# Kernel optimization log

Hardware: AMD Instinct MI355X
Metric: run time of the kernel (lower is better)

The kernel has to match this reference:

```python
import jax, jax.numpy as jnp
import numpy as np
import math

IMAGE_SIZE = 256
N_ANGLES = 180


def setup_inputs() -> dict:
    key = jax.random.key(0)
    x = jax.random.normal(key, (4, 1, IMAGE_SIZE, IMAGE_SIZE), dtype=jnp.float32)
    return {"x": x}


def reference(x) -> jnp.ndarray:
    # Radon transform, circle=True: mask to inscribed circle, then for each
    # angle bilinearly sample the image along rotated coordinates
    # (torch.grid_sample, align_corners=True, zeros padding) and sum along rays.
    B = x.shape[0]
    S = IMAGE_SIZE
    A = N_ANGLES
    img = x.reshape(B, S, S)

    # circular mask (matches torch: sqrt(dist2) <= center with center = S//2)
    center = S // 2
    yy, xx = jnp.meshgrid(jnp.arange(S), jnp.arange(S), indexing='ij')
    dist = jnp.sqrt(((xx - center) ** 2 + (yy - center) ** 2).astype(jnp.float32))
    img = img * (dist <= center).astype(img.dtype)
    img_flat = img.reshape(B, S * S)

    # projection coordinates: meshgrid('ij') of linspace(-S/2, S/2, S)
    lin = jnp.linspace(-S / 2.0, S / 2.0, S, dtype=jnp.float32)
    X, Y = jnp.meshgrid(lin, lin, indexing='ij')  # [S,S]; X varies along i
    Xf, Yf = X.ravel(), Y.ravel()                 # [S*S]

    # all rotation angles at once: torch.linspace(0, 180, A) degrees
    ang = jnp.linspace(0.0, 180.0, A, dtype=jnp.float32) * (math.pi / 180.0)
    c = jnp.cos(ang)[:, None]  # [A,1]
    s = jnp.sin(ang)[:, None]
    half = S / 2.0
    gx = (c * Xf - s * Yf) / half  # [A, S*S], normalized grid x (width)
    gy = (s * Xf + c * Yf) / half  # [A, S*S], normalized grid y (height)

    # align_corners=True: pixel = (g + 1)/2 * (S - 1)
    px = (gx + 1.0) * 0.5 * (S - 1)
    py = (gy + 1.0) * 0.5 * (S - 1)

    x0 = jnp.floor(px)
    y0 = jnp.floor(py)
    wx = px - x0
    wy = py - y0
    x0i = x0.astype(jnp.int32)
    y0i = y0.astype(jnp.int32)
    x1i = x0i + 1
    y1i = y0i + 1

    def corner(xi, yi, w):
        # zeros padding: out-of-bounds corners contribute 0
        valid = (xi >= 0) & (xi < S) & (yi >= 0) & (yi < S)
        idx = jnp.clip(yi, 0, S - 1) * S + jnp.clip(xi, 0, S - 1)  # [A, S*S]
        vals = jnp.take(img_flat, idx, axis=1)                      # [B, A, S*S]
        return vals * (w * valid.astype(img.dtype))

    acc = (corner(x0i, y0i, (1.0 - wx) * (1.0 - wy))
           + corner(x1i, y0i, wx * (1.0 - wy))
           + corner(x0i, y1i, (1.0 - wx) * wy)
           + corner(x1i, y1i, wx * wy))  # [B, A, S*S]

    # flat order is (i, j) from meshgrid('ij'); torch sums over output H == i
    sinogram = acc.reshape(B, A, S, S).sum(axis=2)  # [B, A, S]
    return sinogram
```

## Files before the change

### kernel.cpp

```cpp
#include <hip/hip_runtime.h>
#include <hip/hip_fp16.h>
#include <math.h>

#define S 256
#define A 180
#define B 4
#define PMAX 310
#define NROWS 264

__global__ void radon_mask_f16(const float* __restrict__ in, __half* __restrict__ out) {
    int idx = blockIdx.x * 256 + threadIdx.x;
    int p = idx & (S * S - 1);
    int y = p >> 8;
    int x = p & 255;
    int dx = x - 128, dy = y - 128;
    float v = in[idx];
    v = (dx * dx + dy * dy <= 16384) ? v : 0.0f;
    out[idx] = __float2half(v);
}

__global__ __launch_bounds__(1024, 1) void radon_lds_kernel(const __half* __restrict__ img,
                                                            float* __restrict__ out) {
    __shared__ __half lds[NROWS * PMAX];

    const int a = blockIdx.x;
    const int b = blockIdx.y;
    const int tid = threadIdx.x;

    float ang = (float)a * (float)(M_PI / 179.0);
    float sn, cs;
    sincosf(ang, &sn, &cs);

    int P = 264;
    {
        float best = 1e9f;
        for (int cand = 264; cand <= PMAX; cand += 2) {
            float sd = 0.5f * fabsf((float)cand * cs - sn);
            float m = sd - 2.0f * floorf(sd * 0.5f);
            float score = fabsf(m - 1.0f);
            if (score < best) { best = score; P = cand; }
        }
    }
    const int Ph = P >> 1;

    uint* l32 = (uint*)lds;
    const uint* __restrict__ src = (const uint*)(img + (size_t)b * (S * S));
#pragma unroll
    for (int k = 0; k < 32; ++k) {
        int p = k * 1024 + tid;
        int y = p >> 7;
        int xd = p & 127;
        l32[(y + 4) * Ph + xd + 2] = src[p];
    }
    {
        int rsel = tid >> 7;
        int r = (rsel < 4) ? rsel : (256 + rsel);
        l32[r * Ph + (tid & 127) + 4] = 0u;
        if (tid < 32) {
            int rs = tid >> 2;
            int rr = (rs < 4) ? rs : (256 + rs);
            l32[rr * Ph + (tid & 3)] = 0u;
        }
        int rc = 4 + (tid >> 2);
        int dsel = tid & 3;
        int dd = (dsel < 2) ? dsel : (128 + dsel);
        l32[rc * Ph + dd] = 0u;
    }
    __syncthreads();

    const int j = tid >> 2;
    const int q = tid & 3;

    const float ry = (float)j - 127.5f;
    const float bx = fmaf(-sn, ry, 127.5f);
    const float by = fmaf(cs, ry, 127.5f);
    const float ry2 = ry * ry;

    float h = sqrtf(16934.0f - ry2);
    int ilo = max((int)ceilf(127.5f - h), 0);
    int ihi = min((int)floorf(127.5f + h) + 1, S);
    int len = ihi - ilo;
    int lo = ilo + ((q * len) >> 2);
    int hi = ilo + (((q + 1) * len) >> 2);

    const __half* __restrict__ orig = &lds[4 * P + 4];

    float acc = 0.0f;

#pragma unroll 4
    for (int i = lo; i < hi; ++i) {
        float rx = (float)i - 127.5f;
        float px = fmaf(cs, rx, bx);
        float py = fmaf(sn, rx, by);

        float x0f = floorf(px);
        float y0f = floorf(py);
        float wx = px - x0f;
        float wy = py - y0f;
        int x0 = (int)x0f;
        int y0 = (int)y0f;
        float ux = 1.0f - wx;
        float uy = 1.0f - wy;
        float w00 = ux * uy;
        float w10 = wx * uy;
        float w01 = ux * wy;
        float w11 = wx * wy;

        const __half* p0 = orig + (y0 * P + x0);
        float v00 = __half2float(p0[0]);
        float v10 = __half2float(p0[1]);
        float v01 = __half2float(p0[P]);
        float v11 = __half2float(p0[P + 1]);

        acc = fmaf(w00, v00, fmaf(w10, v10, fmaf(w01, v01, fmaf(w11, v11, acc))));
    }

    __syncthreads();
    float* red = (float*)lds;
    red[tid] = acc;
    __syncthreads();
    if (tid < 256) {
        float4 v = ((const float4*)red)[tid];
        out[((size_t)b * A + a) * S + tid] = v.x + v.y + v.z + v.w;
    }
}

extern "C" void kernel_launch(void* const* d_in, const int* in_sizes, int n_in,
                              void* d_out, int out_size, void* d_ws, size_t ws_size,
                              hipStream_t stream) {
    const float* x = (const float*)d_in[0];
    float* out = (float*)d_out;
    __half* masked = (__half*)d_ws;

    radon_mask_f16<<<dim3((B * S * S) / 256), dim3(256), 0, stream>>>(x, masked);
    radon_lds_kernel<<<dim3(A, B), dim3(1024), 0, stream>>>(masked, out);
}
```

Baseline: 96.03 us.

## Split image into two row halves per block to shrink LDS and raise occupancy

Each (angle, batch) block is split into two blocks along grid z, and each block loads only about half the image rows into LDS. Every ray is cut at the row-128 crossing, each half sums its own segment, and the two partial sums are combined with atomicAdd into an output that the mask kernel now zeroes. The smaller LDS footprint is meant to allow several blocks per CU and to double the grid, hiding load latency. The cost is a full LDS zero-fill pass, the atomics, extra index math, and uneven work between halves at some angles.

```diff
diff --git a/kernel.cpp b/kernel.cpp
--- a/kernel.cpp
+++ b/kernel.cpp
@@ -5,10 +5,11 @@
 #define S 256
 #define A 180
 #define B 4
-#define PMAX 310
-#define NROWS 264
+#define PMAX 296
+#define NR 137
 
-__global__ void radon_mask_f16(const float* __restrict__ in, __half* __restrict__ out) {
+__global__ void radon_mask_f16(const float* __restrict__ in, __half* __restrict__ out,
+                               float* __restrict__ osino) {
     int idx = blockIdx.x * 256 + threadIdx.x;
     int p = idx & (S * S - 1);
     int y = p >> 8;
@@ -17,24 +18,26 @@
     float v = in[idx];
     v = (dx * dx + dy * dy <= 16384) ? v : 0.0f;
     out[idx] = __float2half(v);
+    if (idx < A * B * S) osino[idx] = 0.0f;
 }
 
-__global__ __launch_bounds__(1024, 1) void radon_lds_kernel(const __half* __restrict__ img,
+__global__ __launch_bounds__(1024, 8) void radon_lds_kernel(const __half* __restrict__ img,
                                                             float* __restrict__ out) {
-    __shared__ __half lds[NROWS * PMAX];
+    __shared__ __half lds[NR * PMAX];
 
     const int a = blockIdx.x;
     const int b = blockIdx.y;
+    const int h = blockIdx.z;
     const int tid = threadIdx.x;
 
     float ang = (float)a * (float)(M_PI / 179.0);
     float sn, cs;
     sincosf(ang, &sn, &cs);
 
-    int P = 264;
+    int P = 266;
     {
         float best = 1e9f;
-        for (int cand = 264; cand <= PMAX; cand += 2) {
+        for (int cand = 266; cand <= PMAX; cand += 2) {
             float sd = 0.5f * fabsf((float)cand * cs - sn);
             float m = sd - 2.0f * floorf(sd * 0.5f);
             float score = fabsf(m - 1.0f);
@@ -42,29 +45,31 @@
         }
     }
     const int Ph = P >> 1;
+    const int row0 = h ? 124 : -4;
 
     uint* l32 = (uint*)lds;
-    const uint* __restrict__ src = (const uint*)(img + (size_t)b * (S * S));
+    {
+        int nz = NR * Ph;
 #pragma unroll
-    for (int k = 0; k < 32; ++k) {
-        int p = k * 1024 + tid;
-        int y = p >> 7;
-        int xd = p & 127;
-        l32[(y + 4) * Ph + xd + 2] = src[p];
+        for (int k = 0; k < 20; ++k) {
+            int p = k * 1024 + tid;
+            if (p < nz) l32[p] = 0u;
+        }
     }
+    __syncthreads();
     {
-        int rsel = tid >> 7;
-        int r = (rsel < 4) ? rsel : (256 + rsel);
-        l32[r * Ph + (tid & 127) + 4] = 0u;
-        if (tid < 32) {
-            int rs = tid >> 2;
-            int rr = (rs < 4) ? rs : (256 + rs);
-            l32[rr * Ph + (tid & 3)] = 0u;
+        const int r0img = h ? 124 : 0;
+        const uint* __restrict__ src = (const uint*)(img + (size_t)b * (S * S));
+#pragma unroll
+        for (int k = 0; k < 17; ++k) {
+            int p = k * 1024 + tid;
+            if (p < 132 * 128) {
+                int r = p >> 7;
+                int xd = p & 127;
+                int dstrow = r + (h ? 0 : 4);
+                l32[dstrow * Ph + xd + 2] = src[(r0img + r) * 128 + xd];
+            }
         }
-        int rc = 4 + (tid >> 2);
-        int dsel = tid & 3;
-        int dd = (dsel < 2) ? dsel : (128 + dsel);
-        l32[rc * Ph + dd] = 0u;
     }
     __syncthreads();
 
@@ -76,14 +81,20 @@
     const float by = fmaf(cs, ry, 127.5f);
     const float ry2 = ry * ry;
 
-    float h = sqrtf(16934.0f - ry2);
-    int ilo = max((int)ceilf(127.5f - h), 0);
-    int ihi = min((int)floorf(127.5f + h) + 1, S);
-    int len = ihi - ilo;
-    int lo = ilo + ((q * len) >> 2);
-    int hi = ilo + (((q + 1) * len) >> 2);
+    float hd = sqrtf(16934.0f - ry2);
+    int ilo = max((int)ceilf(127.5f - hd), 0);
+    int ihi = min((int)floorf(127.5f + hd) + 1, S);
 
-    const __half* __restrict__ orig = &lds[4 * P + 4];
+    float tsf = 127.5f + (128.0f - by) / sn;
+    tsf = fminf(fmaxf(tsf, 0.0f), 256.0f);
+    int isplit = (int)ceilf(tsf);
+    int lo0 = h ? max(ilo, isplit) : ilo;
+    int hi0 = h ? ihi : min(ihi, isplit);
+    int len = max(hi0 - lo0, 0);
+    int lo = lo0 + ((q * len) >> 2);
+    int hi = lo0 + (((q + 1) * len) >> 2);
+
+    const int base = -row0 * P + 4;
 
     float acc = 0.0f;
 
@@ -106,7 +117,7 @@
         float w01 = ux * wy;
         float w11 = wx * wy;
 
-        const __half* p0 = orig + (y0 * P + x0);
+        const __half* p0 = &lds[base + y0 * P + x0];
         float v00 = __half2float(p0[0]);
         float v10 = __half2float(p0[1]);
         float v01 = __half2float(p0[P]);
@@ -121,7 +132,7 @@
     __syncthreads();
     if (tid < 256) {
         float4 v = ((const float4*)red)[tid];
-        out[((size_t)b * A + a) * S + tid] = v.x + v.y + v.z + v.w;
+        atomicAdd(&out[((size_t)b * A + a) * S + tid], v.x + v.y + v.z + v.w);
     }
 }
 
@@ -132,6 +143,6 @@
     float* out = (float*)d_out;
     __half* masked = (__half*)d_ws;
 
-    radon_mask_f16<<<dim3((B * S * S) / 256), dim3(256), 0, stream>>>(x, masked);
-    radon_lds_kernel<<<dim3(A, B), dim3(1024), 0, stream>>>(masked, out);
+    radon_mask_f16<<<dim3((B * S * S) / 256), dim3(256), 0, stream>>>(x, masked, out);
+    radon_lds_kernel<<<dim3(A, B, 2), dim3(1024), 0, stream>>>(masked, out);
 }
```

Result: faster. 92.42 us (-3.8%).
